# Kernel optimization log

Hardware: AMD Instinct MI355X
Metric: run time of the kernel (lower is better)

Reference implementation:

```python
import jax, jax.numpy as jnp
import numpy as np

EPS = 1e-12  # matches torch F.normalize default eps


def _l2_normalize(x):
    # F.normalize: x / max(||x||_2, eps), along last dim
    n = jnp.sqrt(jnp.sum(x * x, axis=-1, keepdims=True))
    return x / jnp.maximum(n, EPS)


def setup_inputs() -> dict:
    key = jax.random.key(0)
    k1, k2, k3, k4 = jax.random.split(key, 4)
    N, M, D = 2048, 100000, 256
    return {
        "shape_embedding": jax.random.normal(k1, (N, D), dtype=jnp.float32),
        "gallery_embedding": jax.random.normal(k2, (M, D), dtype=jnp.float32),
        "category_idx": jax.random.randint(k3, (M,), 0, 9, dtype=jnp.int64) if jax.config.jax_enable_x64 else jax.random.randint(k3, (M,), 0, 9, dtype=jnp.int32),
        "shape_idx": jax.random.randint(k4, (M,), 0, 10000, dtype=jnp.int32),
    }


def reference(shape_embedding, gallery_embedding, category_idx, shape_idx):
    # Gallery embeddings are L2-normalized once in __init__; query normalized per call.
    g = _l2_normalize(gallery_embedding)          # [M, D]
    q = _l2_normalize(shape_embedding)            # [N, D]
    scores = jnp.einsum('nd,md->nm', q, g)        # cosine similarity [N, M]
    idx = jnp.argmax(scores, axis=-1)             # top-1 retrieval [N]
    return category_idx[idx], shape_idx[idx]
```

## Files before the change

### kernel.cpp

```cpp
#include <hip/hip_runtime.h>
#include <hip/hip_fp16.h>
#include <math.h>
#include <float.h>

#define M_G 100000
#define M_PAD 100032
#define NT64 1563
#define N_Q 2048
#define DIM 256
#define NG 3126
#define GSTR 3136
#define MARGIN 0.009f

typedef _Float16 f16x8 __attribute__((ext_vector_type(8)));
typedef float f32x16 __attribute__((ext_vector_type(16)));

#define WS_GP 0
#define WS_QP 51216384
#define WS_BM 52264960

__device__ inline unsigned pack_h2(float a, float b) {
    __half ha = __float2half(a), hb = __float2half(b);
    return (unsigned)*(unsigned short*)&ha | ((unsigned)*(unsigned short*)&hb << 16);
}
__device__ inline void gload_lds16(const void* gsrc, void* ldst) {
    __builtin_amdgcn_global_load_lds(
        (const __attribute__((address_space(1))) unsigned int*)gsrc,
        (__attribute__((address_space(3))) unsigned int*)ldst, 16, 0, 0);
}

#define BAR __builtin_amdgcn_s_barrier()
#define LGKM0 { asm volatile("s_waitcnt lgkmcnt(0)" ::: "memory"); \
                __builtin_amdgcn_sched_barrier(0); }
#define VMCNT(n) { asm volatile("s_waitcnt vmcnt(" #n ")" ::: "memory"); \
                   __builtin_amdgcn_sched_barrier(0); }

__global__ __launch_bounds__(256) void pack_kernel(
    const float* __restrict__ g, const float* __restrict__ q,
    uint4* __restrict__ gp, uint4* __restrict__ qp)
{
    const int b = blockIdx.x;
    const int w4 = threadIdx.x >> 6, lane = threadIdx.x & 63;
    const bool isg = b < (M_PAD / 4);
    const int row = (isg ? b : b - M_PAD / 4) * 4 + w4;
    const bool real = !isg || row < M_G;
    const float* src = isg ? g + (size_t)row * DIM : q + (size_t)row * DIM;

    float inv = 0.0f;
    if (real) {
        float4 v = ((const float4*)src)[lane];
        float ss = v.x * v.x + v.y * v.y + v.z * v.z + v.w * v.w;
        #pragma unroll
        for (int o = 32; o; o >>= 1) ss += __shfl_xor(ss, o);
        inv = 1.0f / fmaxf(sqrtf(ss), 1e-12f);
    }
    if (lane < 32) {
        uint4 w = make_uint4(0u, 0u, 0u, 0u);
        if (real) {
            float4 a = ((const float4*)src)[lane * 2];
            float4 c = ((const float4*)src)[lane * 2 + 1];
            w.x = pack_h2(a.x * inv, a.y * inv);
            w.y = pack_h2(a.z * inv, a.w * inv);
            w.z = pack_h2(c.x * inv, c.y * inv);
            w.w = pack_h2(c.z * inv, c.w * inv);
        }
        const int kt = lane >> 3, gg = lane & 7;
        if (isg) {
            int mt = row >> 6, rl = row & 63;
            gp[((size_t)mt * 4 + kt) * 512 + rl * 8 + (gg ^ (rl & 7))] = w;
        } else {
            int qt = row >> 8, rl = row & 255;
            qp[((size_t)qt * 4 + kt) * 2048 + rl * 8 + (gg ^ (rl & 7))] = w;
        }
    }
}

#define STAGE32(dstbase, src) { const uint4* s_ = (src); _Pragma("unroll") \
  for (int p_ = 0; p_ < 4; ++p_) \
    gload_lds16(s_ + p_ * 512 + tid, lds + (dstbase) + (p_ * 512 + tid) * 16); }

#define READ_BQ(KT, bufbase) { _Pragma("unroll") \
  for (int sl_ = 0; sl_ < 4; ++sl_) { _Pragma("unroll") \
    for (int cb_ = 0; cb_ < 2; ++cb_) \
      bR[(KT) * 4 + sl_][cb_] = *(const f16x8*)(lds + (bufbase) + qroff + \
          cb_ * 4096 + ((((sl_ << 1) + lh) ^ l7) << 4)); } }

#define RD_A(S) (*(const f16x8*)(pb + ((S) >> 2) * 8192 + \
    ((((((S) & 3) << 1) + lh) ^ l7) << 4)))

#define MFMA32(AV, S) { \
    acc[0] = __builtin_amdgcn_mfma_f32_32x32x16_f16(AV, bR[S][0], acc[0], 0, 0, 0); \
    acc[1] = __builtin_amdgcn_mfma_f32_32x32x16_f16(AV, bR[S][1], acc[1], 0, 0, 0); }
#define MFMB32(AV, S) { \
    accb[0] = __builtin_amdgcn_mfma_f32_32x32x16_f16(AV, bR[S][0], accb[0], 0, 0, 0); \
    accb[1] = __builtin_amdgcn_mfma_f32_32x32x16_f16(AV, bR[S][1], accb[1], 0, 0, 0); }

__global__ __launch_bounds__(512, 2) void scoreA_kernel(
    const uint4* __restrict__ gp, const uint4* __restrict__ qp,
    unsigned short* __restrict__ bmaxH)
{
    extern __shared__ char lds[];

    const int bid = blockIdx.x;
    const int xcd = bid & 7;
    const int qt = (bid >> 3) & 7;
    const int mc = (bid >> 6) * 8 + xcd;
    const int nt = (mc < 27) ? 25 : 24;
    const int t0 = (mc < 27) ? mc * 25 : 675 + (mc - 27) * 24;

    const int tid = threadIdx.x;
    const int wid = tid >> 6, lane = tid & 63;
    const int wr = wid >> 2, wc = wid & 3;
    const int l31 = lane & 31, lh = lane >> 5, l7 = lane & 7;
    const int qroff = (wc * 64 + l31) * 128;
    const int aroff = (wr * 32 + l31) * 128;

    const uint4* qsrc = qp + (size_t)qt * 8192;

    f16x8 bR[16][2];
    STAGE32(0,     qsrc + 0 * 2048);
    STAGE32(32768, qsrc + 1 * 2048);
    VMCNT(4); BAR;
    READ_BQ(0, 0); LGKM0; BAR;
    STAGE32(0, qsrc + 2 * 2048);
    VMCNT(4); BAR;
    READ_BQ(1, 32768); LGKM0; BAR;
    STAGE32(32768, qsrc + 3 * 2048);
    VMCNT(4); BAR;
    READ_BQ(2, 0); LGKM0; BAR;
    STAGE32(0, gp + (size_t)t0 * 2048);
    VMCNT(4); BAR;
    READ_BQ(3, 32768); LGKM0; BAR;
    VMCNT(0); BAR;

    for (int t = 0; t < nt; ++t) {
        const int mtile = t0 + t;
        const int cur = (t & 1) << 15;
        const int nxt = cur ^ 32768;
        if (t + 1 < nt) STAGE32(nxt, gp + (size_t)(mtile + 1) * 2048);

        f32x16 acc[2], accb[2];
        #pragma unroll
        for (int c = 0; c < 2; ++c)
            #pragma unroll
            for (int i = 0; i < 16; ++i) { acc[c][i] = 0.f; accb[c][i] = 0.f; }

        const char* pb = lds + cur + aroff;
        f16x8 aP, aQ;
        aP = RD_A(0);
        #pragma unroll
        for (int sp = 0; sp < 8; ++sp) {
            aQ = RD_A(2 * sp + 1);
            MFMA32(aP, 2 * sp);
            if (sp < 7) aP = RD_A(2 * sp + 2);
            MFMB32(aQ, 2 * sp + 1);
        }

        const int group = mtile * 2 + wr;
        const bool padgrp = (mtile * 64 + wr * 32) >= M_G;
        #pragma unroll
        for (int cb = 0; cb < 2; ++cb) {
            f32x16 f = acc[cb] + accb[cb];
            float m0 = fmaxf(fmaxf(fmaxf(f[0], f[1]), fmaxf(f[2], f[3])),
                             fmaxf(fmaxf(f[4], f[5]), fmaxf(f[6], f[7])));
            float m1 = fmaxf(fmaxf(fmaxf(f[8], f[9]), fmaxf(f[10], f[11])),
                             fmaxf(fmaxf(f[12], f[13]), fmaxf(f[14], f[15])));
            float v = fmaxf(m0, m1);
            v = fmaxf(v, __shfl_xor(v, 32));
            if (lane < 32) {
                int qn = qt * 256 + wc * 64 + cb * 32 + l31;
                __half h = __float2half(padgrp ? -65504.f : v);
                bmaxH[(size_t)qn * GSTR + group] = *(unsigned short*)&h;
            }
        }
        if (t + 1 < nt) { VMCNT(2); BAR; }
    }
}

__global__ __launch_bounds__(256) void phaseB_kernel(
    const float* __restrict__ q, const float* __restrict__ g,
    const unsigned short* __restrict__ bmaxH,
    const int* __restrict__ cat, const int* __restrict__ shp,
    int* __restrict__ out)
{
    __shared__ __align__(16) float qrow[DIM];
    __shared__ int glist[NG];
    __shared__ int ng;
    __shared__ float smax[4];
    __shared__ float rbs[4];
    __shared__ int rbi[4];

    const int qi = blockIdx.x;
    const int tid = threadIdx.x;
    const int lane = tid & 63, wid = tid >> 6;
    const __half* bm = (const __half*)(bmaxH + (size_t)qi * GSTR);
    if (tid < 64)
        *(float4*)&qrow[tid * 4] = *(const float4*)(q + (size_t)qi * DIM + tid * 4);
    if (tid == 0) ng = 0;

    float m = -FLT_MAX;
    for (int gr = tid; gr < NG; gr += 256)
        m = fmaxf(m, __half2float(bm[gr]));
    #pragma unroll
    for (int o = 32; o; o >>= 1) m = fmaxf(m, __shfl_xor(m, o));
    if (lane == 0) smax[wid] = m;
    __syncthreads();
    const float thr = fmaxf(fmaxf(smax[0], smax[1]), fmaxf(smax[2], smax[3])) - MARGIN;

    for (int gr = tid; gr < NG; gr += 256)
        if (__half2float(bm[gr]) >= thr)
            glist[atomicAdd(&ng, 1)] = gr;
    __syncthreads();

    float bs = -FLT_MAX;
    int bi = 0x7fffffff;
    const int r = tid >> 3, p = tid & 7;
    const int n = ng;
    for (int i = 0; i < n; ++i) {
        int mm = glist[i] * 32 + r;
        if (mm < M_G) {
            const float* grow = g + (size_t)mm * DIM + p * 32;
            const float* qr = qrow + p * 32;
            float s = 0.f, ssq = 0.f;
            #pragma unroll
            for (int jj = 0; jj < 8; ++jj) {
                float4 gv = *(const float4*)(grow + jj * 4);
                float4 qv = *(const float4*)(qr + jj * 4);
                s += gv.x * qv.x + gv.y * qv.y + gv.z * qv.z + gv.w * qv.w;
                ssq += gv.x * gv.x + gv.y * gv.y + gv.z * gv.z + gv.w * gv.w;
            }
            s += __shfl_xor(s, 1);  s += __shfl_xor(s, 2);  s += __shfl_xor(s, 4);
            ssq += __shfl_xor(ssq, 1); ssq += __shfl_xor(ssq, 2); ssq += __shfl_xor(ssq, 4);
            s *= 1.0f / fmaxf(sqrtf(ssq), 1e-12f);
            if (p == 0 && (s > bs || (s == bs && mm < bi))) { bs = s; bi = mm; }
        }
    }
    #pragma unroll
    for (int o = 1; o < 64; o <<= 1) {
        float os = __shfl_xor(bs, o);
        int oi = __shfl_xor(bi, o);
        if (os > bs || (os == bs && oi < bi)) { bs = os; bi = oi; }
    }
    if (lane == 0) { rbs[wid] = bs; rbi[wid] = bi; }
    __syncthreads();
    if (tid == 0) {
        #pragma unroll
        for (int ww = 1; ww < 4; ++ww)
            if (rbs[ww] > bs || (rbs[ww] == bs && rbi[ww] < bi)) { bs = rbs[ww]; bi = rbi[ww]; }
        out[qi] = cat[bi];
        out[N_Q + qi] = shp[bi];
    }
}

extern "C" void kernel_launch(void* const* d_in, const int* in_sizes, int n_in,
                              void* d_out, int out_size, void* d_ws, size_t ws_size,
                              hipStream_t stream) {
    const float* q = (const float*)d_in[0];
    const float* g = (const float*)d_in[1];
    const int* cat = (const int*)d_in[2];
    const int* shp = (const int*)d_in[3];
    int* out = (int*)d_out;

    char* ws = (char*)d_ws;
    uint4* gp             = (uint4*)(ws + WS_GP);
    uint4* qp             = (uint4*)(ws + WS_QP);
    unsigned short* bmaxH = (unsigned short*)(ws + WS_BM);

    hipFuncSetAttribute((const void*)scoreA_kernel,
                        hipFuncAttributeMaxDynamicSharedMemorySize, 65536);

    pack_kernel<<<M_PAD / 4 + N_Q / 4, 256, 0, stream>>>(g, q, gp, qp);
    scoreA_kernel<<<512, 512, 65536, stream>>>(gp, qp, bmaxH);
    phaseB_kernel<<<N_Q, 256, 0, stream>>>(q, g, bmaxH, cat, shp, out);
}
```

Before: 170.6 us.

## Interleave staged prefetch with MFMA phases using barriers and setprio in scoreA

Splits the per-tile MFMA loop into four phases. Each phase reads four A fragments from LDS ahead of use and issues one quarter of the next tile's global-to-LDS prefetch. Phases are separated by workgroup barriers, with s_setprio raised around the MFMA bursts. The goal is to spread memory traffic across the compute instead of issuing it all up front, and to keep waves on a SIMD alternating between memory and math. The cost is extra barriers per tile and higher register pressure from holding eight fragments, which could reduce occupancy or add stall time.

```diff
diff --git a/kernel.cpp b/kernel.cpp
--- a/kernel.cpp
+++ b/kernel.cpp
@@ -31,6 +31,8 @@
 
 #define BAR __builtin_amdgcn_s_barrier()
 #define LGKM0 { asm volatile("s_waitcnt lgkmcnt(0)" ::: "memory"); \
+                __builtin_amdgcn_sched_barrier(0); }
+#define LGKM4 { asm volatile("s_waitcnt lgkmcnt(4)" ::: "memory"); \
                 __builtin_amdgcn_sched_barrier(0); }
 #define VMCNT(n) { asm volatile("s_waitcnt vmcnt(" #n ")" ::: "memory"); \
                    __builtin_amdgcn_sched_barrier(0); }
@@ -79,6 +81,9 @@
   for (int p_ = 0; p_ < 4; ++p_) \
     gload_lds16(s_ + p_ * 512 + tid, lds + (dstbase) + (p_ * 512 + tid) * 16); }
 
+#define STAGE_P(dstbase, src, P) { const uint4* s_ = (src); \
+    gload_lds16(s_ + (P) * 512 + tid, lds + (dstbase) + ((P) * 512 + tid) * 16); }
+
 #define READ_BQ(KT, bufbase) { _Pragma("unroll") \
   for (int sl_ = 0; sl_ < 4; ++sl_) { _Pragma("unroll") \
     for (int cb_ = 0; cb_ < 2; ++cb_) \
@@ -137,7 +142,8 @@
         const int mtile = t0 + t;
         const int cur = (t & 1) << 15;
         const int nxt = cur ^ 32768;
-        if (t + 1 < nt) STAGE32(nxt, gp + (size_t)(mtile + 1) * 2048);
+        const uint4* nsrc = gp + (size_t)(mtile + 1) * 2048;
+        const bool pf = (t + 1 < nt);
 
         f32x16 acc[2], accb[2];
         #pragma unroll
@@ -146,15 +152,38 @@
             for (int i = 0; i < 16; ++i) { acc[c][i] = 0.f; accb[c][i] = 0.f; }
 
         const char* pb = lds + cur + aroff;
-        f16x8 aP, aQ;
-        aP = RD_A(0);
-        #pragma unroll
-        for (int sp = 0; sp < 8; ++sp) {
-            aQ = RD_A(2 * sp + 1);
-            MFMA32(aP, 2 * sp);
-            if (sp < 7) aP = RD_A(2 * sp + 2);
-            MFMB32(aQ, 2 * sp + 1);
-        }
+        f16x8 pA0, pA1, pA2, pA3;
+        f16x8 pN0, pN1, pN2, pN3;
+
+        pA0 = RD_A(0);  pA1 = RD_A(1);  pA2 = RD_A(2);  pA3 = RD_A(3);
+
+        pN0 = RD_A(4);  pN1 = RD_A(5);  pN2 = RD_A(6);  pN3 = RD_A(7);
+        if (pf) STAGE_P(nxt, nsrc, 0);
+        BAR; LGKM4;
+        __builtin_amdgcn_s_setprio(1);
+        MFMA32(pA0, 0); MFMB32(pA1, 1); MFMA32(pA2, 2); MFMB32(pA3, 3);
+        __builtin_amdgcn_s_setprio(0);
+        BAR;
+        pA0 = RD_A(8);  pA1 = RD_A(9);  pA2 = RD_A(10); pA3 = RD_A(11);
+        if (pf) STAGE_P(nxt, nsrc, 1);
+        BAR; LGKM4;
+        __builtin_amdgcn_s_setprio(1);
+        MFMA32(pN0, 4); MFMB32(pN1, 5); MFMA32(pN2, 6); MFMB32(pN3, 7);
+        __builtin_amdgcn_s_setprio(0);
+        BAR;
+        pN0 = RD_A(12); pN1 = RD_A(13); pN2 = RD_A(14); pN3 = RD_A(15);
+        if (pf) STAGE_P(nxt, nsrc, 2);
+        BAR; LGKM4;
+        __builtin_amdgcn_s_setprio(1);
+        MFMA32(pA0, 8); MFMB32(pA1, 9); MFMA32(pA2, 10); MFMB32(pA3, 11);
+        __builtin_amdgcn_s_setprio(0);
+        BAR;
+        if (pf) STAGE_P(nxt, nsrc, 3);
+        BAR; LGKM0;
+        __builtin_amdgcn_s_setprio(1);
+        MFMA32(pN0, 12); MFMB32(pN1, 13); MFMA32(pN2, 14); MFMB32(pN3, 15);
+        __builtin_amdgcn_s_setprio(0);
+        BAR;
 
         const int group = mtile * 2 + wr;
         const bool padgrp = (mtile * 64 + wr * 32) >= M_G;
@@ -173,7 +202,7 @@
                 bmaxH[(size_t)qn * GSTR + group] = *(unsigned short*)&h;
             }
         }
-        if (t + 1 < nt) { VMCNT(2); BAR; }
+        if (pf) { VMCNT(2); BAR; }
     }
 }
 
```

Result: slower. 176.9 us (+3.7%).
